# Kernel optimization log

Hardware: AMD Instinct MI355X
Metric: run time of the kernel (lower is better)

## Reference

```python
import jax, jax.numpy as jnp
import numpy as np

N = 100000        # num nodes
E = 1600000       # num edges (avg degree 16)
IN_DIM = 256
OUT_DIM = 64
NEG_SLOPE = 0.2
EPS = 1e-9


def setup_inputs() -> dict:
    key = jax.random.key(0)
    k1, k2, k3, k4 = jax.random.split(key, 4)
    node_features = jax.random.normal(k1, (N, IN_DIM), dtype=jnp.float32)
    edge_index = jax.random.randint(k2, (2, E), 0, N, dtype=jnp.int32)
    # learned params (xavier-ish scale)
    W = jax.random.normal(k3, (OUT_DIM, IN_DIM), dtype=jnp.float32) * (1.0 / np.sqrt(IN_DIM))
    attn = jax.random.normal(k4, (2 * OUT_DIM,), dtype=jnp.float32) * (1.0 / np.sqrt(2 * OUT_DIM))
    bias = jnp.zeros((OUT_DIM,), dtype=jnp.float32)
    return {"node_features": node_features, "edge_index": edge_index,
            "W": W, "attn": attn, "bias": bias}


def reference(node_features, edge_index, W, attn, bias):
    # h = linear(node_features)  [N, D]
    h = node_features @ W.T
    src, dst = edge_index[0], edge_index[1]
    # (cat(h_src, h_dst) * attn).sum(-1) == h_src @ attn[:D] + h_dst @ attn[D:]
    a_src = h @ attn[:OUT_DIM]   # [N]
    a_dst = h @ attn[OUT_DIM:]   # [N]
    e = a_src[src] + a_dst[dst]  # [E]
    e = jnp.where(e >= 0, e, NEG_SLOPE * e)  # leaky_relu
    # segment softmax over dst
    max_per_dst = jax.ops.segment_max(e, dst, num_segments=N)       # [N]
    exp_scores = jnp.exp(e - max_per_dst[dst])                       # [E]
    sum_per_dst = jax.ops.segment_sum(exp_scores, dst, num_segments=N)
    attention = exp_scores / (sum_per_dst[dst] + EPS)                # [E]
    # dropout: p=0 / eval mode -> identity
    msg = attention[:, None] * h[src]                                 # [E, D]
    out = jax.ops.segment_sum(msg, dst, num_segments=N)              # [N, D]
    return out + bias
```

## Files before the change

### kernel.cpp

```cpp
#include <hip/hip_runtime.h>
#include <math.h>

#define IN_DIM 256
#define OUT_DIM 64
#define NEG_SLOPE 0.2f
#define EPS_GAT 1e-9f

__global__ __launch_bounds__(128) void gat_k1_linear(
    const float* __restrict__ X, const float* __restrict__ W,
    const float* __restrict__ attn, float* __restrict__ h,
    float* __restrict__ a_s, float* __restrict__ a_d, int N)
{
    __shared__ float sX[32 * 132];
    __shared__ float sW[32 * 68];

    const int tid = threadIdx.x;
    const int tx = tid & 7;
    const int ty = tid >> 3;
    const int n0 = blockIdx.x * 128;

    const float4* X4 = (const float4*)X;
    const float4* W4 = (const float4*)W;

    float acc[8][8];
    #pragma unroll
    for (int i = 0; i < 8; ++i)
        #pragma unroll
        for (int j = 0; j < 8; ++j) acc[i][j] = 0.f;

    float as_r[8], ad_r[8];
    #pragma unroll
    for (int j = 0; j < 8; ++j) {
        as_r[j] = attn[tx * 8 + j];
        ad_r[j] = attn[OUT_DIM + tx * 8 + j];
    }

    const int xc4 = tid & 7;
    const int xr0 = tid >> 3;

    for (int k0 = 0; k0 < IN_DIM; k0 += 32) {
        const int k0c4 = k0 >> 2;
        __syncthreads();
        #pragma unroll
        for (int p = 0; p < 8; ++p) {
            const int row = p * 16 + xr0;
            int n = n0 + row; if (n >= N) n = N - 1;
            float4 v = X4[(size_t)n * 64 + k0c4 + xc4];
            const int kb = xc4 * 4;
            sX[(kb + 0) * 132 + row] = v.x;
            sX[(kb + 1) * 132 + row] = v.y;
            sX[(kb + 2) * 132 + row] = v.z;
            sX[(kb + 3) * 132 + row] = v.w;
        }
        #pragma unroll
        for (int p = 0; p < 4; ++p) {
            const int idx = p * 128 + tid;
            const int o = idx >> 3, c4 = idx & 7;
            float4 v = W4[(size_t)o * 64 + k0c4 + c4];
            const int kb = c4 * 4;
            sW[(kb + 0) * 68 + o] = v.x;
            sW[(kb + 1) * 68 + o] = v.y;
            sW[(kb + 2) * 68 + o] = v.z;
            sW[(kb + 3) * 68 + o] = v.w;
        }
        __syncthreads();
        #pragma unroll 2
        for (int kk = 0; kk < 32; ++kk) {
            const float4* xp = (const float4*)&sX[kk * 132 + ty * 8];
            const float4* wp = (const float4*)&sW[kk * 68 + tx * 8];
            float4 xa = xp[0], xb = xp[1];
            float4 wa = wp[0], wb = wp[1];
            float xv[8] = {xa.x, xa.y, xa.z, xa.w, xb.x, xb.y, xb.z, xb.w};
            float wv[8] = {wa.x, wa.y, wa.z, wa.w, wb.x, wb.y, wb.z, wb.w};
            #pragma unroll
            for (int i = 0; i < 8; ++i)
                #pragma unroll
                for (int j = 0; j < 8; ++j) acc[i][j] += xv[i] * wv[j];
        }
    }

    float4* h4 = (float4*)h;
    #pragma unroll
    for (int m = 0; m < 8; ++m) {
        const int n = n0 + ty * 8 + m;
        float vs = 0.f, vd = 0.f;
        #pragma unroll
        for (int j = 0; j < 8; ++j) { vs += acc[m][j] * as_r[j]; vd += acc[m][j] * ad_r[j]; }
        vs += __shfl_xor(vs, 1); vs += __shfl_xor(vs, 2); vs += __shfl_xor(vs, 4);
        vd += __shfl_xor(vd, 1); vd += __shfl_xor(vd, 2); vd += __shfl_xor(vd, 4);
        if (n < N) {
            float4 lo = {acc[m][0], acc[m][1], acc[m][2], acc[m][3]};
            float4 hi = {acc[m][4], acc[m][5], acc[m][6], acc[m][7]};
            h4[(size_t)n * 16 + tx * 2]     = lo;
            h4[(size_t)n * 16 + tx * 2 + 1] = hi;
            if (tx == 0) { a_s[n] = vs; a_d[n] = vd; }
        }
    }
}

__global__ __launch_bounds__(256) void gat_k2_hist(
    const int* __restrict__ dst, int* __restrict__ counts, int E)
{
    for (int i = blockIdx.x * 256 + threadIdx.x; i < E; i += gridDim.x * 256)
        atomicAdd(&counts[dst[i]], 1);
}

__global__ __launch_bounds__(1024) void gat_k3_scan(
    const int* __restrict__ counts, int* __restrict__ offsets,
    int* __restrict__ allocCursor, int N)
{
    __shared__ int wsum[16];
    __shared__ int blockBase;
    const int n = blockIdx.x * 1024 + threadIdx.x;
    const int lane = threadIdx.x & 63;
    const int wave = threadIdx.x >> 6;
    const int v = (n < N) ? counts[n] : 0;
    int incl = v;
    #pragma unroll
    for (int off = 1; off < 64; off <<= 1) {
        int t = __shfl_up(incl, off);
        if (lane >= off) incl += t;
    }
    if (lane == 63) wsum[wave] = incl;
    __syncthreads();
    if (wave == 0) {
        int wv = (lane < 16) ? wsum[lane] : 0;
        int wincl = wv;
        #pragma unroll
        for (int off = 1; off < 16; off <<= 1) {
            int t = __shfl_up(wincl, off);
            if (lane >= off) wincl += t;
        }
        if (lane < 16) wsum[lane] = wincl - wv;
        if (lane == 15) blockBase = atomicAdd(allocCursor, wincl);
    }
    __syncthreads();
    if (n < N) offsets[n] = blockBase + wsum[wave] + (incl - v);
}

__global__ __launch_bounds__(256) void gat_k4_scatter(
    const int* __restrict__ src, const int* __restrict__ dst,
    const float* __restrict__ a_s, const float* __restrict__ a_d,
    const int* __restrict__ offsets, int* __restrict__ cursor,
    int2* __restrict__ packed, int E)
{
    for (int i = blockIdx.x * 256 + threadIdx.x; i < E; i += gridDim.x * 256) {
        const int s = src[i], d = dst[i];
        float e = a_s[s] + a_d[d];
        e = (e >= 0.f) ? e : NEG_SLOPE * e;
        const int pos = offsets[d] + atomicAdd(&cursor[d], 1);
        packed[pos] = make_int2(s, __float_as_int(e));
    }
}

__global__ __launch_bounds__(256) void gat_k5_aggregate(
    const float* __restrict__ h, const int2* __restrict__ packed,
    const int* __restrict__ offsets, const int* __restrict__ counts,
    const float* __restrict__ bias, float* __restrict__ out, int N)
{
    const int wave = threadIdx.x >> 6, lane = threadIdx.x & 63;
    const int d = blockIdx.x * 4 + wave;
    if (d >= N) return;
    const int deg = counts[d], base = offsets[d];
    const int slot = lane >> 4, q = lane & 15;
    const float4* h4 = (const float4*)h;

    float4 acc = {0.f, 0.f, 0.f, 0.f};

    if (deg <= 64) {
        int s = 0; float e = -INFINITY;
        if (lane < deg) { int2 pe = packed[base + lane]; s = pe.x; e = __int_as_float(pe.y); }
        float m = e;
        #pragma unroll
        for (int off = 32; off; off >>= 1) m = fmaxf(m, __shfl_xor(m, off));
        float p = (lane < deg) ? __expf(e - m) : 0.f;
        float sum = p;
        #pragma unroll
        for (int off = 32; off; off >>= 1) sum += __shfl_xor(sum, off);
        const float w = p / (sum + EPS_GAT);
        for (int t0 = 0; t0 < deg; t0 += 4) {
            const float wg = __shfl(w, t0 + slot);
            const int  sid = __shfl(s, t0 + slot);
            float4 hv = h4[(size_t)sid * 16 + q];
            acc.x += wg * hv.x; acc.y += wg * hv.y;
            acc.z += wg * hv.z; acc.w += wg * hv.w;
        }
    } else {
        float m = -INFINITY;
        for (int j = lane; j < deg; j += 64)
            m = fmaxf(m, __int_as_float(packed[base + j].y));
        #pragma unroll
        for (int off = 32; off; off >>= 1) m = fmaxf(m, __shfl_xor(m, off));
        float sum = 0.f;
        for (int j = lane; j < deg; j += 64)
            sum += __expf(__int_as_float(packed[base + j].y) - m);
        #pragma unroll
        for (int off = 32; off; off >>= 1) sum += __shfl_xor(sum, off);
        const float inv = 1.f / (sum + EPS_GAT);
        for (int j0 = 0; j0 < deg; j0 += 64) {
            int s = 0; float w = 0.f;
            if (j0 + lane < deg) {
                int2 pe = packed[base + j0 + lane];
                s = pe.x;
                w = __expf(__int_as_float(pe.y) - m) * inv;
            }
            const int cnt = min(64, deg - j0);
            for (int t0 = 0; t0 < cnt; t0 += 4) {
                const float wg = __shfl(w, t0 + slot);
                const int  sid = __shfl(s, t0 + slot);
                float4 hv = h4[(size_t)sid * 16 + q];
                acc.x += wg * hv.x; acc.y += wg * hv.y;
                acc.z += wg * hv.z; acc.w += wg * hv.w;
            }
        }
    }

    acc.x += __shfl_xor(acc.x, 16); acc.x += __shfl_xor(acc.x, 32);
    acc.y += __shfl_xor(acc.y, 16); acc.y += __shfl_xor(acc.y, 32);
    acc.z += __shfl_xor(acc.z, 16); acc.z += __shfl_xor(acc.z, 32);
    acc.w += __shfl_xor(acc.w, 16); acc.w += __shfl_xor(acc.w, 32);

    if (slot == 0) {
        const float4* b4 = (const float4*)bias;
        float4 bv = b4[q];
        float4 o;
        o.x = acc.x + bv.x; o.y = acc.y + bv.y;
        o.z = acc.z + bv.z; o.w = acc.w + bv.w;
        ((float4*)out)[(size_t)d * 16 + q] = o;
    }
}

extern "C" void kernel_launch(void* const* d_in, const int* in_sizes, int n_in,
                              void* d_out, int out_size, void* d_ws, size_t ws_size,
                              hipStream_t stream)
{
    const float* X    = (const float*)d_in[0];
    const int*   EI   = (const int*)d_in[1];
    const float* W    = (const float*)d_in[2];
    const float* attn = (const float*)d_in[3];
    const float* bias = (const float*)d_in[4];
    float* out = (float*)d_out;

    const int N = in_sizes[0] / IN_DIM;
    const int E = in_sizes[1] / 2;
    const int* src = EI;
    const int* dst = EI + E;

    char* ws = (char*)d_ws;
    float* h      = (float*)ws; ws += (size_t)N * OUT_DIM * sizeof(float);
    float* a_s    = (float*)ws; ws += (size_t)N * sizeof(float);
    float* a_d    = (float*)ws; ws += (size_t)N * sizeof(float);
    int*   counts = (int*)ws;   ws += (size_t)N * sizeof(int);
    int*   cursor = (int*)ws;   ws += (size_t)N * sizeof(int);
    int*   alloc  = (int*)ws;   ws += 256;
    int*   offsets= (int*)ws;   ws += (size_t)N * sizeof(int);
    int2*  packed = (int2*)ws;  ws += (size_t)E * sizeof(int2);

    hipMemsetAsync(counts, 0, (size_t)(2 * N) * sizeof(int) + 256, stream);

    gat_k1_linear<<<(N + 127) / 128, 128, 0, stream>>>(X, W, attn, h, a_s, a_d, N);
    gat_k2_hist<<<2048, 256, 0, stream>>>(dst, counts, E);
    gat_k3_scan<<<(N + 1023) / 1024, 1024, 0, stream>>>(counts, offsets, alloc, N);
    gat_k4_scatter<<<2048, 256, 0, stream>>>(src, dst, a_s, a_d, offsets, cursor,
                                             packed, E);
    gat_k5_aggregate<<<(N + 3) / 4, 256, 0, stream>>>(h, packed, offsets, counts,
                                                      bias, out, N);
}
```

Before: 413.1 us.

## Store only sorted src in CSR scatter, recompute edge scores in aggregate

The scatter kernel now writes only the source index per edge, no longer the packed (src, score) pair. It bumps the offsets array directly, which drops the separate cursor array and the offsets read. The aggregate kernel recomputes the leaky-relu score from a_s[src] + a_d[dst] and recovers the segment base as offsets minus degree. The histogram and scatter kernels read dst and src as int4 with halved grids, which shrinks the intermediate edge buffer and the memset. In exchange, aggregate does extra gathers into a_s, and in the high-degree path the score is recomputed up to three times.

New measurement: 445.3 us. 1.08x slower.

```diff
diff --git a/kernel.cpp b/kernel.cpp
--- a/kernel.cpp
+++ b/kernel.cpp
@@ -101,7 +101,18 @@
 __global__ __launch_bounds__(256) void gat_k2_hist(
     const int* __restrict__ dst, int* __restrict__ counts, int E)
 {
-    for (int i = blockIdx.x * 256 + threadIdx.x; i < E; i += gridDim.x * 256)
+    const int gtid = blockIdx.x * 256 + threadIdx.x;
+    const int gsz  = gridDim.x * 256;
+    const int E4 = E >> 2;
+    const int4* d4 = (const int4*)dst;
+    for (int i = gtid; i < E4; i += gsz) {
+        int4 v = d4[i];
+        atomicAdd(&counts[v.x], 1);
+        atomicAdd(&counts[v.y], 1);
+        atomicAdd(&counts[v.z], 1);
+        atomicAdd(&counts[v.w], 1);
+    }
+    for (int i = (E4 << 2) + gtid; i < E; i += gsz)
         atomicAdd(&counts[dst[i]], 1);
 }
 
@@ -140,28 +151,37 @@
 
 __global__ __launch_bounds__(256) void gat_k4_scatter(
     const int* __restrict__ src, const int* __restrict__ dst,
+    int* __restrict__ offsets, int* __restrict__ sorted_src, int E)
+{
+    const int gtid = blockIdx.x * 256 + threadIdx.x;
+    const int gsz  = gridDim.x * 256;
+    const int E4 = E >> 2;
+    const int4* s4 = (const int4*)src;
+    const int4* d4 = (const int4*)dst;
+    for (int i = gtid; i < E4; i += gsz) {
+        int4 s = s4[i];
+        int4 d = d4[i];
+        sorted_src[atomicAdd(&offsets[d.x], 1)] = s.x;
+        sorted_src[atomicAdd(&offsets[d.y], 1)] = s.y;
+        sorted_src[atomicAdd(&offsets[d.z], 1)] = s.z;
+        sorted_src[atomicAdd(&offsets[d.w], 1)] = s.w;
+    }
+    for (int i = (E4 << 2) + gtid; i < E; i += gsz)
+        sorted_src[atomicAdd(&offsets[dst[i]], 1)] = src[i];
+}
+
+__global__ __launch_bounds__(256) void gat_k5_aggregate(
+    const float* __restrict__ h, const int* __restrict__ sorted_src,
+    const int* __restrict__ offsets, const int* __restrict__ counts,
     const float* __restrict__ a_s, const float* __restrict__ a_d,
-    const int* __restrict__ offsets, int* __restrict__ cursor,
-    int2* __restrict__ packed, int E)
-{
-    for (int i = blockIdx.x * 256 + threadIdx.x; i < E; i += gridDim.x * 256) {
-        const int s = src[i], d = dst[i];
-        float e = a_s[s] + a_d[d];
-        e = (e >= 0.f) ? e : NEG_SLOPE * e;
-        const int pos = offsets[d] + atomicAdd(&cursor[d], 1);
-        packed[pos] = make_int2(s, __float_as_int(e));
-    }
-}
-
-__global__ __launch_bounds__(256) void gat_k5_aggregate(
-    const float* __restrict__ h, const int2* __restrict__ packed,
-    const int* __restrict__ offsets, const int* __restrict__ counts,
     const float* __restrict__ bias, float* __restrict__ out, int N)
 {
     const int wave = threadIdx.x >> 6, lane = threadIdx.x & 63;
     const int d = blockIdx.x * 4 + wave;
     if (d >= N) return;
-    const int deg = counts[d], base = offsets[d];
+    const int deg  = counts[d];
+    const int base = offsets[d] - deg;
+    const float ad = a_d[d];
     const int slot = lane >> 4, q = lane & 15;
     const float4* h4 = (const float4*)h;
 
@@ -169,7 +189,11 @@
 
     if (deg <= 64) {
         int s = 0; float e = -INFINITY;
-        if (lane < deg) { int2 pe = packed[base + lane]; s = pe.x; e = __int_as_float(pe.y); }
+        if (lane < deg) {
+            s = sorted_src[base + lane];
+            e = a_s[s] + ad;
+            e = (e >= 0.f) ? e : NEG_SLOPE * e;
+        }
         float m = e;
         #pragma unroll
         for (int off = 32; off; off >>= 1) m = fmaxf(m, __shfl_xor(m, off));
@@ -187,22 +211,29 @@
         }
     } else {
         float m = -INFINITY;
-        for (int j = lane; j < deg; j += 64)
-            m = fmaxf(m, __int_as_float(packed[base + j].y));
+        for (int j = lane; j < deg; j += 64) {
+            float e = a_s[sorted_src[base + j]] + ad;
+            e = (e >= 0.f) ? e : NEG_SLOPE * e;
+            m = fmaxf(m, e);
+        }
         #pragma unroll
         for (int off = 32; off; off >>= 1) m = fmaxf(m, __shfl_xor(m, off));
         float sum = 0.f;
-        for (int j = lane; j < deg; j += 64)
-            sum += __expf(__int_as_float(packed[base + j].y) - m);
+        for (int j = lane; j < deg; j += 64) {
+            float e = a_s[sorted_src[base + j]] + ad;
+            e = (e >= 0.f) ? e : NEG_SLOPE * e;
+            sum += __expf(e - m);
+        }
         #pragma unroll
         for (int off = 32; off; off >>= 1) sum += __shfl_xor(sum, off);
         const float inv = 1.f / (sum + EPS_GAT);
         for (int j0 = 0; j0 < deg; j0 += 64) {
             int s = 0; float w = 0.f;
             if (j0 + lane < deg) {
-                int2 pe = packed[base + j0 + lane];
-                s = pe.x;
-                w = __expf(__int_as_float(pe.y) - m) * inv;
+                s = sorted_src[base + j0 + lane];
+                float e = a_s[s] + ad;
+                e = (e >= 0.f) ? e : NEG_SLOPE * e;
+                w = __expf(e - m) * inv;
             }
             const int cnt = min(64, deg - j0);
             for (int t0 = 0; t0 < cnt; t0 += 4) {
@@ -251,18 +282,16 @@
     float* a_s    = (float*)ws; ws += (size_t)N * sizeof(float);
     float* a_d    = (float*)ws; ws += (size_t)N * sizeof(float);
     int*   counts = (int*)ws;   ws += (size_t)N * sizeof(int);
-    int*   cursor = (int*)ws;   ws += (size_t)N * sizeof(int);
     int*   alloc  = (int*)ws;   ws += 256;
     int*   offsets= (int*)ws;   ws += (size_t)N * sizeof(int);
-    int2*  packed = (int2*)ws;  ws += (size_t)E * sizeof(int2);
-
-    hipMemsetAsync(counts, 0, (size_t)(2 * N) * sizeof(int) + 256, stream);
+    int*   sorted_src = (int*)ws; ws += (size_t)E * sizeof(int);
+
+    hipMemsetAsync(counts, 0, (size_t)N * sizeof(int) + 256, stream);
 
     gat_k1_linear<<<(N + 127) / 128, 128, 0, stream>>>(X, W, attn, h, a_s, a_d, N);
-    gat_k2_hist<<<2048, 256, 0, stream>>>(dst, counts, E);
+    gat_k2_hist<<<1024, 256, 0, stream>>>(dst, counts, E);
     gat_k3_scan<<<(N + 1023) / 1024, 1024, 0, stream>>>(counts, offsets, alloc, N);
-    gat_k4_scatter<<<2048, 256, 0, stream>>>(src, dst, a_s, a_d, offsets, cursor,
-                                             packed, E);
-    gat_k5_aggregate<<<(N + 3) / 4, 256, 0, stream>>>(h, packed, offsets, counts,
-                                                      bias, out, N);
-}
+    gat_k4_scatter<<<1024, 256, 0, stream>>>(src, dst, offsets, sorted_src, E);
+    gat_k5_aggregate<<<(N + 3) / 4, 256, 0, stream>>>(h, sorted_src, offsets, counts,
+                                                      a_s, a_d, bias, out, N);
+}
```
